# Optimization experiments

Hardware: AMD Instinct MI355X
Metric: run time of the kernel (lower is better)

The kernel has to match this reference:

```python
import jax, jax.numpy as jnp
import numpy as np
import math

N_HEADS = 8
SLOPE = 0.01      # LeakyReLU negative slope (torch default)
EPS_K = 1e-6      # numerical stabilizer in softmax kernel transformation
EPS_N = 1e-5      # GraphNorm eps
TAU = 1.0
N_NODES = 50000
DIM = 64          # in = hidden = out channels (head dim)
M_FEAT = 30       # nb_random_features
N_EDGES = 800000


def softmax_kernel(data, proj, is_query):
    # data: [N, H, D], proj: [M, D] -> [N, H, M] positive random features
    dn = 1.0 / math.sqrt(math.sqrt(data.shape[-1]))
    ratio = 1.0 / math.sqrt(proj.shape[0])
    dd = jnp.einsum('nhd,md->nhm', dn * data, proj)
    diag = jnp.sum(jnp.square(data), axis=-1, keepdims=True) * (dn * dn * 0.5)
    if is_query:
        stab = jnp.max(dd, axis=-1, keepdims=True)            # per (n,h)
    else:
        stab = jnp.max(dd, axis=(0, 2), keepdims=True)        # per h, over n and m
    return ratio * (jnp.exp(dd - diag - stab) + EPS_K)


def nodeformer_conv(x, Wq, bq, Wk, bk, Wv, bv, Wo, bo, proj):
    # x: [N, C]; Wq/Wk/Wv: [C, H*D]; Wo: [H*D, D_out]; proj: [M, D]
    N = x.shape[0]
    H = N_HEADS
    D = Wq.shape[1] // H
    inv = 1.0 / math.sqrt(TAU)
    q = ((x @ Wq + bq).reshape(N, H, D)) * inv
    k = ((x @ Wk + bk).reshape(N, H, D)) * inv
    v = (x @ Wv + bv).reshape(N, H, D)
    qp = softmax_kernel(q, proj, True)    # [N,H,M]
    kp = softmax_kernel(k, proj, False)   # [N,H,M]
    kvs = jnp.einsum('nhm,nhd->hmd', kp, v)          # O(N) linear attention
    num = jnp.einsum('nhm,hmd->nhd', qp, kvs)
    den = jnp.einsum('nhm,hm->nh', qp, jnp.sum(kp, axis=0))
    z = num / den[..., None]                          # [N,H,D]
    return z.reshape(N, H * D) @ Wo + bo


def graph_norm(x, gamma, beta, alpha):
    # single graph: normalize over all nodes; alpha = learnable mean scale
    mu = jnp.mean(x, axis=0, keepdims=True)
    xc = x - alpha * mu
    var = jnp.mean(jnp.square(xc), axis=0, keepdims=True)
    return gamma * xc * jax.lax.rsqrt(var + EPS_N) + beta


def leaky_relu(x):
    return jnp.where(x >= 0, x, SLOPE * x)


def setup_inputs() -> dict:
    key = jax.random.key(0)
    ks = jax.random.split(key, 12)
    HD = N_HEADS * DIM
    s = 0.02
    inp = {
        'patch_embs': jax.random.normal(ks[0], (N_NODES, DIM), jnp.float32),
        'edge_index': jax.random.randint(ks[1], (2, N_EDGES), 0, N_NODES),
        'edge_attr': jax.random.normal(ks[2], (N_EDGES, 8), jnp.float32),
        'Wq': jax.random.normal(ks[3], (3, DIM, HD), jnp.float32) * s,
        'Wk': jax.random.normal(ks[4], (3, DIM, HD), jnp.float32) * s,
        'Wv': jax.random.normal(ks[5], (3, DIM, HD), jnp.float32) * s,
        'Wo': jax.random.normal(ks[6], (3, HD, DIM), jnp.float32) * s,
        'bq': jnp.zeros((3, HD), jnp.float32),
        'bk': jnp.zeros((3, HD), jnp.float32),
        'bv': jnp.zeros((3, HD), jnp.float32),
        'bo': jnp.zeros((3, DIM), jnp.float32),
        'P': jax.random.normal(ks[7], (3, M_FEAT, DIM), jnp.float32),
        'gamma': jnp.ones((3, DIM), jnp.float32),
        'beta': jnp.zeros((3, DIM), jnp.float32),
        'alpha': jnp.ones((3, DIM), jnp.float32),
    }
    return inp


def reference(patch_embs, edge_index, edge_attr, Wq, Wk, Wv, Wo, bq, bk, bv, bo, P, gamma, beta, alpha):
    x = nodeformer_conv(patch_embs, Wq[0], bq[0], Wk[0], bk[0], Wv[0], bv[0], Wo[0], bo[0], P[0])
    x = graph_norm(leaky_relu(x), gamma[0], beta[0], alpha[0])
    x = nodeformer_conv(x, Wq[1], bq[1], Wk[1], bk[1], Wv[1], bv[1], Wo[1], bo[1], P[1])
    x = graph_norm(leaky_relu(x), gamma[1], beta[1], alpha[1])
    x = nodeformer_conv(x, Wq[2], bq[2], Wk[2], bk[2], Wv[2], bv[2], Wo[2], bo[2], P[2])
    x = graph_norm(x, gamma[2], beta[2], alpha[2])
    return x
```

## Files before the change

kernel.cpp:

```cpp
#include <hip/hip_runtime.h>
#include <math.h>


namespace {

constexpr int N    = 50000;
constexpr int C    = 64;
constexpr int H    = 8;
constexpr int HD   = 512;
constexpr int M    = 30;

constexpr int NBK  = 128;
constexpr int NGK  = N / 16;
constexpr int NBQ  = 1024;
constexpr int NGQ8 = N / 8;
constexpr int PSTR = 2016;

__device__ constexpr double DN    = 0.35355339059327373;
__device__ constexpr double RATIO = 0.18257418583505536;
__device__ constexpr double EPSK  = 1e-6;
__device__ constexpr double EPSN  = 1e-5;

__device__ __forceinline__ void kah(double& s, double& c, double v) {
  double y = v - c; double t = s + y; c = (t - s) - y; s = t;
}

__global__ __launch_bounds__(256)
void k_wp(const float* __restrict__ Wk, const float* __restrict__ bk,
          const float* __restrict__ Wq, const float* __restrict__ bq,
          const float* __restrict__ P, float* __restrict__ wp,
          float* __restrict__ bp) {
  const int blk = blockIdx.x, side = blk >> 3, h = blk & 7, t = threadIdx.x;
  const float* W  = side ? Wq : Wk;
  const float* bb = side ? bq : bk;
  for (int s = t; s < 1920; s += 256) {
    const int m = s >> 6, c = s & 63;
    double a = 0.0;
    for (int d = 0; d < 64; ++d)
      a = fma((double)W[c * HD + h * 64 + d], (double)P[m * 64 + d], a);
    wp[((size_t)(side * 8 + h) * 30 + m) * 64 + c] = (float)(a * DN);
  }
  if (t < 30) {
    double a = 0.0;
    for (int d = 0; d < 64; ++d)
      a = fma((double)bb[h * 64 + d], (double)P[t * 64 + d], a);
    bp[(side * 8 + h) * 30 + t] = (float)(a * DN);
  }
}

__global__ __launch_bounds__(256, 4)
void k_kv(const float* __restrict__ x32,
          const float* __restrict__ Wk, const float* __restrict__ bk,
          const float* __restrict__ Wv, const float* __restrict__ bv,
          const float* __restrict__ wp, const float* __restrict__ bp,
          float* __restrict__ partial) {
  __shared__ __align__(16) float wvs[4096];
  __shared__ __align__(16) float wpk[30 * 68];
  __shared__ __align__(16) float xs[16 * 68];
  __shared__ __align__(16) float vsd[16 * 68];
  __shared__ float kplV[480];
  __shared__ float diag[16];
  __shared__ float bpk[30];
  const int t = threadIdx.x, i0 = t >> 6, c0 = t & 63;
  const int h = blockIdx.x >> 7, b = blockIdx.x & (NBK - 1), hb = h * 64;

  for (int s = t; s < 4096; s += 256)
    wvs[s] = Wv[(s >> 6) * HD + hb + (s & 63)];
  for (int s = t; s < 1920; s += 256)
    wpk[(s >> 6) * 68 + (s & 63)] = wp[(size_t)h * 1920 + s];
  if (t < 30) bpk[t] = bp[h * 30 + t];
  const float bk0 = bk[hb + c0], bv0 = bv[hb + c0];
  float acc8[8];
#pragma unroll
  for (int k = 0; k < 8; ++k) acc8[k] = 0.0f;
  float ssv = 0.0f, ses = 0.0f, runmax = -3.0e38f;
  __syncthreads();

  for (int g = b; g < NGK; g += NBK) {
    const int n0 = g * 16;
    __syncthreads();
#pragma unroll
    for (int u = 0; u < 4; ++u)
      xs[(i0 + 4 * u) * 68 + c0] = x32[(size_t)(n0 + i0 + 4 * u) * C + c0];
    __syncthreads();
    float ka[4], va[4];
#pragma unroll
    for (int u = 0; u < 4; ++u) { ka[u] = bk0; va[u] = bv0; }
#pragma unroll 4
    for (int c4 = 0; c4 < 16; ++c4) {
      float4 xv[4];
#pragma unroll
      for (int u = 0; u < 4; ++u)
        xv[u] = reinterpret_cast<const float4*>(xs + (i0 + 4 * u) * 68)[c4];
#pragma unroll
      for (int j = 0; j < 4; ++j) {
        const int c = c4 * 4 + j;
        const float wk_ = Wk[c * HD + hb + c0];
        const float wv_ = wvs[c * 64 + c0];
        const float xj0 = (j == 0) ? xv[0].x : (j == 1) ? xv[0].y : (j == 2) ? xv[0].z : xv[0].w;
        const float xj1 = (j == 0) ? xv[1].x : (j == 1) ? xv[1].y : (j == 2) ? xv[1].z : xv[1].w;
        const float xj2 = (j == 0) ? xv[2].x : (j == 1) ? xv[2].y : (j == 2) ? xv[2].z : xv[2].w;
        const float xj3 = (j == 0) ? xv[3].x : (j == 1) ? xv[3].y : (j == 2) ? xv[3].z : xv[3].w;
        ka[0] = fmaf(xj0, wk_, ka[0]); va[0] = fmaf(xj0, wv_, va[0]);
        ka[1] = fmaf(xj1, wk_, ka[1]); va[1] = fmaf(xj1, wv_, va[1]);
        ka[2] = fmaf(xj2, wk_, ka[2]); va[2] = fmaf(xj2, wv_, va[2]);
        ka[3] = fmaf(xj3, wk_, ka[3]); va[3] = fmaf(xj3, wv_, va[3]);
      }
    }
#pragma unroll
    for (int u = 0; u < 4; ++u) {
      vsd[(i0 + 4 * u) * 68 + c0] = va[u];
      float s = ka[u] * ka[u];
#pragma unroll
      for (int off = 32; off; off >>= 1) s += __shfl_xor(s, off, 64);
      if (c0 == 0) diag[i0 + 4 * u] = s * 0.0625f;
      ssv += va[u];
    }
    __syncthreads();
#pragma unroll
    for (int rep = 0; rep < 2; ++rep) {
      const int item = t + rep * 256;
      if (item < 480) {
        const int di = item / 30, dm = item - di * 30;
        float a = bpk[dm];
#pragma unroll 4
        for (int c4 = 0; c4 < 16; ++c4) {
          const float4 xv = reinterpret_cast<const float4*>(xs + di * 68)[c4];
          const float4 wv = reinterpret_cast<const float4*>(wpk + dm * 68)[c4];
          a = fmaf(xv.x, wv.x, a); a = fmaf(xv.y, wv.y, a);
          a = fmaf(xv.z, wv.z, a); a = fmaf(xv.w, wv.w, a);
        }
        runmax = fmaxf(runmax, a);
        kplV[item] = __expf(a - diag[di]);
      }
    }
    __syncthreads();
    if (t < 30) {
      float gsum = 0.0f;
#pragma unroll
      for (int i = 0; i < 16; ++i) gsum += kplV[i * 30 + t];
      ses += gsum;
    }
    float vr[16];
#pragma unroll
    for (int i = 0; i < 16; ++i) vr[i] = vsd[i * 68 + c0];
#pragma unroll
    for (int k = 0; k < 8; ++k) {
      const int s = t + (k << 8);
      if (s < 1920) {
        const int m = s >> 6;
        float gsum = acc8[k];
#pragma unroll
        for (int i = 0; i < 16; ++i)
          gsum = fmaf(kplV[i * 30 + m], vr[i], gsum);
        acc8[k] = gsum;
      }
    }
  }
  const size_t base = (size_t)blockIdx.x * PSTR;
  __syncthreads();
  xs[t] = ssv;
  vsd[t] = runmax;
  __syncthreads();
  if (t < 64) partial[base + 1950 + t] = xs[t] + xs[t + 64] + xs[t + 128] + xs[t + 192];
  for (int off = 128; off; off >>= 1) {
    if (t < off) vsd[t] = fmaxf(vsd[t], vsd[t + off]);
    __syncthreads();
  }
  if (t == 0) partial[base + 2014] = vsd[0];
  if (t < 30) partial[base + 1920 + t] = ses;
#pragma unroll
  for (int k = 0; k < 8; ++k) {
    const int s = t + (k << 8);
    if (s < 1920) partial[base + s] = acc8[k];
  }
}

__global__ __launch_bounds__(256)
void k_redkv(const float* __restrict__ partial, const float* __restrict__ Wo,
             double* __restrict__ ksumg, float* __restrict__ Gg32) {
  const int h = blockIdx.x, t = threadIdx.x;
  __shared__ float red[256];
  __shared__ double svt[64];
  __shared__ double kvls[M * 64];
  __shared__ double escs;
  const size_t hb = (size_t)h * NBK;
  red[t] = (t < NBK) ? partial[(hb + t) * PSTR + 2014] : -3.0e38f;
  __syncthreads();
  for (int off = 128; off; off >>= 1) {
    if (t < off) red[t] = fmaxf(red[t], red[t + off]);
    __syncthreads();
  }
  if (t == 0) escs = exp(-(double)red[0]);
  __syncthreads();
  const double esc = escs;
  if (t < 64) {
    double s = 0.0;
    for (int b = 0; b < NBK; ++b) s += (double)partial[(hb + b) * PSTR + 1950 + t];
    svt[t] = s;
  } else if (t < 64 + M) {
    const int m = t - 64;
    double s = 0.0;
    for (int b = 0; b < NBK; ++b) s += (double)partial[(hb + b) * PSTR + 1920 + m];
    ksumg[h * M + m] = RATIO * (esc * s + EPSK * (double)N);
  }
  __syncthreads();
#pragma unroll
  for (int k = 0; k < 8; ++k) {
    const int sidx = t + (k << 8);
    if (sidx < M * 64) {
      double s = 0.0;
      for (int b = 0; b < NBK; ++b) s += (double)partial[(hb + b) * PSTR + sidx];
      kvls[sidx] = RATIO * (esc * s + EPSK * svt[sidx & 63]);
    }
  }
  __syncthreads();
#pragma unroll
  for (int k = 0; k < 8; ++k) {
    const int sidx = t + (k << 8);
    if (sidx < M * 64) {
      const int m = sidx >> 6, c = sidx & 63;
      double a = 0.0;
      for (int d = 0; d < 64; ++d)
        a = fma(kvls[m * 64 + d], (double)Wo[(h * 64 + d) * 64 + c], a);
      Gg32[(size_t)h * 1920 + sidx] = (float)a;
    }
  }
}

template <int MODE>
__global__ __launch_bounds__(256, 4)
void k_q(const float* __restrict__ x32,
         const float* __restrict__ Wq, const float* __restrict__ bq,
         const float* __restrict__ wp, const float* __restrict__ bp,
         const double* __restrict__ ksumg, const float* __restrict__ Gg32,
         const float* __restrict__ bo, int do_leaky, int H0,
         double* __restrict__ y, double* __restrict__ psum) {
  __shared__ __align__(16) float wpq[2][30 * 68];
  __shared__ float Gl[2][1920];
  __shared__ __align__(16) float xs[8 * 68];
  __shared__ float qpl[480];
  __shared__ float stabd[16], diagd[16];
  __shared__ double ksl[2][30];
  __shared__ double rdend[16];
  __shared__ float bpq2[2][30];
  __shared__ double red[256];
  const int t = threadIdx.x, i0 = t >> 6, c0 = t & 63;

  for (int s = t; s < 3840; s += 256) {
    const int hh = s / 1920, r = s - hh * 1920, m = r >> 6, c = r & 63;
    wpq[hh][m * 68 + c] = wp[(size_t)(8 + H0 + hh) * 1920 + r];
    Gl[hh][r] = Gg32[(size_t)(H0 + hh) * 1920 + r];
  }
  if (t < 60) {
    ksl[t / 30][t % 30]  = ksumg[(H0 + t / 30) * 30 + (t % 30)];
    bpq2[t / 30][t % 30] = bp[(8 + H0 + t / 30) * 30 + (t % 30)];
  }
  const float bqA = bq[H0 * 64 + c0];
  const float bqB = bq[H0 * 64 + 64 + c0];
  const double bo0 = (double)bo[c0];
  double sy = 0.0, sy2 = 0.0;
  __syncthreads();

  for (int g = blockIdx.x; g < NGQ8; g += NBQ) {
    const int n0 = g * 8;
    __syncthreads();
    xs[i0 * 68 + c0]       = x32[(size_t)(n0 + i0) * C + c0];
    xs[(i0 + 4) * 68 + c0] = x32[(size_t)(n0 + i0 + 4) * C + c0];
    __syncthreads();
    float aq0 = bqA, aq1 = bqB, aq2 = bqA, aq3 = bqB;
#pragma unroll 4
    for (int c4 = 0; c4 < 16; ++c4) {
      const float4 xa = reinterpret_cast<const float4*>(xs + i0 * 68)[c4];
      const float4 xb = reinterpret_cast<const float4*>(xs + (i0 + 4) * 68)[c4];
#pragma unroll
      for (int j = 0; j < 4; ++j) {
        const int c = c4 * 4 + j;
        const float wA = Wq[c * HD + H0 * 64 + c0];
        const float wB = Wq[c * HD + H0 * 64 + 64 + c0];
        const float xaj = (j == 0) ? xa.x : (j == 1) ? xa.y : (j == 2) ? xa.z : xa.w;
        const float xbj = (j == 0) ? xb.x : (j == 1) ? xb.y : (j == 2) ? xb.z : xb.w;
        aq0 = fmaf(xaj, wA, aq0); aq1 = fmaf(xaj, wB, aq1);
        aq2 = fmaf(xbj, wA, aq2); aq3 = fmaf(xbj, wB, aq3);
      }
    }
    {
      float s0 = aq0 * aq0, s1 = aq1 * aq1, s2 = aq2 * aq2, s3 = aq3 * aq3;
#pragma unroll
      for (int off = 32; off; off >>= 1) {
        s0 += __shfl_xor(s0, off, 64); s1 += __shfl_xor(s1, off, 64);
        s2 += __shfl_xor(s2, off, 64); s3 += __shfl_xor(s3, off, 64);
      }
      if (c0 == 0) {
        diagd[i0 * 2]           = s0 * 0.0625f;
        diagd[i0 * 2 + 1]       = s1 * 0.0625f;
        diagd[(i0 + 4) * 2]     = s2 * 0.0625f;
        diagd[(i0 + 4) * 2 + 1] = s3 * 0.0625f;
      }
    }
#pragma unroll
    for (int rep = 0; rep < 2; ++rep) {
      const int item = t + rep * 256;
      if (item < 480) {
        const int i = item / 60, r = item - i * 60, hh = r / 30, m = r - hh * 30;
        float a = bpq2[hh][m];
#pragma unroll 4
        for (int c4 = 0; c4 < 16; ++c4) {
          const float4 xv = reinterpret_cast<const float4*>(xs + i * 68)[c4];
          const float4 wv = reinterpret_cast<const float4*>(wpq[hh] + m * 68)[c4];
          a = fmaf(xv.x, wv.x, a); a = fmaf(xv.y, wv.y, a);
          a = fmaf(xv.z, wv.z, a); a = fmaf(xv.w, wv.w, a);
        }
        qpl[item] = a;
      }
    }
    __syncthreads();
    if (t < 16) {
      const float* q = qpl + t * 30;
      float mx = q[0];
      for (int m = 1; m < 30; ++m) mx = fmaxf(mx, q[m]);
      stabd[t] = mx;
    }
    __syncthreads();
#pragma unroll
    for (int rep = 0; rep < 2; ++rep) {
      const int item = t + rep * 256;
      if (item < 480) {
        const int ih = item / 30;
        qpl[item] = 0.18257418583505536f *
                    (__expf((qpl[item] - diagd[ih]) - stabd[ih]) + 1e-6f);
      }
    }
    __syncthreads();
    if (t < 16) {
      double den = 0.0;
      const float* q = qpl + t * 30;
      const double* ks = ksl[t & 1];
      for (int m = 0; m < 30; ++m) den = fma((double)q[m], ks[m], den);
      rdend[t] = 1.0 / den;
    }
    __syncthreads();
    double acc_a = 0.0, acc_b = 0.0;
#pragma unroll
    for (int hh = 0; hh < 2; ++hh) {
      const float* qa = qpl + (i0 * 2 + hh) * 30;
      const float* qb = qpl + ((i0 + 4) * 2 + hh) * 30;
      const float* g  = Gl[hh] + c0;
      double sa = 0.0, sb = 0.0;
      for (int m = 0; m < 30; ++m) {
        const double gv = (double)g[m * 64];
        sa = fma((double)qa[m], gv, sa);
        sb = fma((double)qb[m], gv, sb);
      }
      acc_a = fma(sa, rdend[i0 * 2 + hh], acc_a);
      acc_b = fma(sb, rdend[(i0 + 4) * 2 + hh], acc_b);
    }
    const size_t ia = (size_t)(n0 + i0) * C + c0;
    const size_t ib = (size_t)(n0 + i0 + 4) * C + c0;
    if (MODE == 0) {
      y[ia] = bo0 + acc_a;
      y[ib] = bo0 + acc_b;
    } else if (MODE == 1) {
      y[ia] += acc_a;
      y[ib] += acc_b;
    } else {
      double va = y[ia] + acc_a, vb = y[ib] + acc_b;
      if (do_leaky) {
        va = (va >= 0.0) ? va : 0.01 * va;
        vb = (vb >= 0.0) ? vb : 0.01 * vb;
      }
      y[ia] = va; y[ib] = vb;
      sy += va + vb;
      sy2 = fma(va, va, sy2);
      sy2 = fma(vb, vb, sy2);
    }
  }
  if (MODE == 2) {
    __syncthreads();
    red[t] = sy;
    __syncthreads();
    if (t < 64) psum[(size_t)blockIdx.x * 128 + t] =
        red[t] + red[t + 64] + red[t + 128] + red[t + 192];
    __syncthreads();
    red[t] = sy2;
    __syncthreads();
    if (t < 64) psum[(size_t)blockIdx.x * 128 + 64 + t] =
        red[t] + red[t + 64] + red[t + 128] + red[t + 192];
  }
}

__global__ void k_norm_params(const double* __restrict__ psum,
                              const float* __restrict__ gamma, const float* __restrict__ beta,
                              const float* __restrict__ alpha, double* __restrict__ nparam) {
  const int t = threadIdx.x;
  __shared__ double m1l[64], m2l[64];
  if (t < 64) {
    double s = 0, c = 0;
    for (int b = 0; b < NBQ; ++b) kah(s, c, psum[(size_t)b * 128 + t]);
    m1l[t] = s - c;
  } else if (t < 128) {
    const int ci = t - 64;
    double s = 0, c = 0;
    for (int b = 0; b < NBQ; ++b) kah(s, c, psum[(size_t)b * 128 + 64 + ci]);
    m2l[ci] = s - c;
  }
  __syncthreads();
  if (t < 64) {
    const double mu = m1l[t] / (double)N;
    const double m2 = m2l[t] / (double)N;
    const double al = (double)alpha[t];
    double var = m2 - (2.0 * al - al * al) * mu * mu;
    if (var < 0.0) var = 0.0;
    nparam[t]       = al * mu;
    nparam[64 + t]  = (double)gamma[t] / sqrt(var + EPSN);
    nparam[128 + t] = (double)beta[t];
  }
}

__global__ void k_cast(const double* __restrict__ yv, const double* __restrict__ nparam,
                       float* __restrict__ dst) {
  const int total = N * C;
  for (int i = blockIdx.x * blockDim.x + threadIdx.x; i < total; i += gridDim.x * blockDim.x) {
    const int c = i & 63;
    dst[i] = (float)((yv[i] - nparam[c]) * nparam[64 + c] + nparam[128 + c]);
  }
}

}

extern "C" void kernel_launch(void* const* d_in, const int* in_sizes, int n_in,
                              void* d_out, int out_size, void* d_ws, size_t ws_size,
                              hipStream_t stream) {
  const float* patch = (const float*)d_in[0];
  const float* Wq = (const float*)d_in[3];
  const float* Wk = (const float*)d_in[4];
  const float* Wv = (const float*)d_in[5];
  const float* Wo = (const float*)d_in[6];
  const float* bq = (const float*)d_in[7];
  const float* bk = (const float*)d_in[8];
  const float* bv = (const float*)d_in[9];
  const float* bo = (const float*)d_in[10];
  const float* P  = (const float*)d_in[11];
  const float* ga = (const float*)d_in[12];
  const float* be = (const float*)d_in[13];
  const float* al = (const float*)d_in[14];
  float* out = (float*)d_out;

  char* wsb = (char*)d_ws;
  double* y      = (double*)wsb;   wsb += (size_t)N * C * 8;
  double* psum   = (double*)wsb;   wsb += (size_t)NBQ * 128 * 8;
  double* nparam = (double*)wsb;   wsb += 192 * 8;
  double* ksumg  = (double*)wsb;   wsb += (size_t)H * M * 8;
  float*  x32    = (float*)wsb;    wsb += (size_t)N * C * 4;
  float*  partial= (float*)wsb;    wsb += (size_t)(H * NBK) * PSTR * 4;
  float*  G32    = (float*)wsb;    wsb += (size_t)H * M * 64 * 4;
  float*  wpf    = (float*)wsb;    wsb += (size_t)2 * H * M * 64 * 4;
  float*  bpf    = (float*)wsb;    wsb += (size_t)2 * H * M * 4;

  for (int L = 0; L < 3; ++L) {
    const float* wq  = Wq + (size_t)L * C * HD;
    const float* wk  = Wk + (size_t)L * C * HD;
    const float* wv  = Wv + (size_t)L * C * HD;
    const float* wo  = Wo + (size_t)L * HD * C;
    const float* bq_ = bq + (size_t)L * HD;
    const float* bk_ = bk + (size_t)L * HD;
    const float* bv_ = bv + (size_t)L * HD;
    const float* bo_ = bo + (size_t)L * C;
    const float* p   = P  + (size_t)L * M * C;
    const int leaky = (L < 2) ? 1 : 0;
    const float* xcur = (L == 0) ? patch : x32;

    k_wp<<<16, 256, 0, stream>>>(wk, bk_, wq, bq_, p, wpf, bpf);
    k_kv<<<H * NBK, 256, 0, stream>>>(xcur, wk, bk_, wv, bv_, wpf, bpf, partial);
    k_redkv<<<H, 256, 0, stream>>>(partial, wo, ksumg, G32);

    k_q<0><<<NBQ, 256, 0, stream>>>(xcur, wq, bq_, wpf, bpf, ksumg, G32, bo_,
                                    leaky, 0, y, psum);
    k_q<1><<<NBQ, 256, 0, stream>>>(xcur, wq, bq_, wpf, bpf, ksumg, G32, bo_,
                                    leaky, 2, y, psum);
    k_q<1><<<NBQ, 256, 0, stream>>>(xcur, wq, bq_, wpf, bpf, ksumg, G32, bo_,
                                    leaky, 4, y, psum);
    k_q<2><<<NBQ, 256, 0, stream>>>(xcur, wq, bq_, wpf, bpf, ksumg, G32, bo_,
                                    leaky, 6, y, psum);

    k_norm_params<<<1, 128, 0, stream>>>(psum, ga + (size_t)L * C, be + (size_t)L * C,
                                         al + (size_t)L * C, nparam);
    k_cast<<<512, 256, 0, stream>>>(y, nparam, (L < 2) ? x32 : out);
  }
}
```

Measured before the change: 2.293 ms.

## Process four heads per query pass and transpose feature buffers in shared memory

The query kernel now handles four heads per launch instead of two, so each layer needs two query launches rather than four and re-reads x and y less often. The MODE 1 accumulate-only path is removed, and MODE 1 now does the final add, optional leaky ReLU and statistics. The G matrix is read straight from global memory instead of being staged in LDS, and the reduction buffer reuses the wpq array, which frees shared memory for the larger four-head projection weights. The random-feature buffers in both kernels are transposed to an m-major layout with unit stride across nodes, which changes LDS access patterns. The cost is higher register pressure from eight accumulators and uncached global G reads inside the inner loop.

```diff
diff --git a/kernel.cpp b/kernel.cpp
--- a/kernel.cpp
+++ b/kernel.cpp
@@ -58,7 +58,7 @@
   __shared__ __align__(16) float wpk[30 * 68];
   __shared__ __align__(16) float xs[16 * 68];
   __shared__ __align__(16) float vsd[16 * 68];
-  __shared__ float kplV[480];
+  __shared__ float kplV[30 * 16];
   __shared__ float diag[16];
   __shared__ float bpk[30];
   const int t = threadIdx.x, i0 = t >> 6, c0 = t & 63;
@@ -121,7 +121,7 @@
     for (int rep = 0; rep < 2; ++rep) {
       const int item = t + rep * 256;
       if (item < 480) {
-        const int di = item / 30, dm = item - di * 30;
+        const int dm = item >> 4, di = item & 15;
         float a = bpk[dm];
 #pragma unroll 4
         for (int c4 = 0; c4 < 16; ++c4) {
@@ -131,14 +131,14 @@
           a = fmaf(xv.z, wv.z, a); a = fmaf(xv.w, wv.w, a);
         }
         runmax = fmaxf(runmax, a);
-        kplV[item] = __expf(a - diag[di]);
+        kplV[dm * 16 + di] = __expf(a - diag[di]);
       }
     }
     __syncthreads();
     if (t < 30) {
       float gsum = 0.0f;
 #pragma unroll
-      for (int i = 0; i < 16; ++i) gsum += kplV[i * 30 + t];
+      for (int i = 0; i < 16; ++i) gsum += kplV[t * 16 + i];
       ses += gsum;
     }
     float vr[16];
@@ -152,7 +152,7 @@
         float gsum = acc8[k];
 #pragma unroll
         for (int i = 0; i < 16; ++i)
-          gsum = fmaf(kplV[i * 30 + m], vr[i], gsum);
+          gsum = fmaf(kplV[m * 16 + i], vr[i], gsum);
         acc8[k] = gsum;
       }
     }
@@ -236,39 +236,39 @@
          const double* __restrict__ ksumg, const float* __restrict__ Gg32,
          const float* __restrict__ bo, int do_leaky, int H0,
          double* __restrict__ y, double* __restrict__ psum) {
-  __shared__ __align__(16) float wpq[2][30 * 68];
-  __shared__ float Gl[2][1920];
+  __shared__ __align__(16) float wpq[4 * 30 * 68];
   __shared__ __align__(16) float xs[8 * 68];
-  __shared__ float qpl[480];
-  __shared__ float stabd[16], diagd[16];
-  __shared__ double ksl[2][30];
-  __shared__ double rdend[16];
-  __shared__ float bpq2[2][30];
-  __shared__ double red[256];
+  __shared__ float  qpl[120 * 8];
+  __shared__ float  stabd[32];
+  __shared__ float  diagd[32];
+  __shared__ double rdend[32];
+  __shared__ double ksl[120];
+  __shared__ float  bpq[120];
   const int t = threadIdx.x, i0 = t >> 6, c0 = t & 63;
 
-  for (int s = t; s < 3840; s += 256) {
-    const int hh = s / 1920, r = s - hh * 1920, m = r >> 6, c = r & 63;
-    wpq[hh][m * 68 + c] = wp[(size_t)(8 + H0 + hh) * 1920 + r];
-    Gl[hh][r] = Gg32[(size_t)(H0 + hh) * 1920 + r];
-  }
-  if (t < 60) {
-    ksl[t / 30][t % 30]  = ksumg[(H0 + t / 30) * 30 + (t % 30)];
-    bpq2[t / 30][t % 30] = bp[(8 + H0 + t / 30) * 30 + (t % 30)];
-  }
-  const float bqA = bq[H0 * 64 + c0];
-  const float bqB = bq[H0 * 64 + 64 + c0];
+  for (int s = t; s < 7680; s += 256) {
+    const int hh = s / 1920, r = s - hh * 1920;
+    wpq[(hh * 30 + (r >> 6)) * 68 + (r & 63)] = wp[(size_t)(8 + H0 + hh) * 1920 + r];
+  }
+  if (t < 120) {
+    ksl[t] = ksumg[H0 * 30 + t];
+    bpq[t] = bp[(8 + H0) * 30 + t];
+  }
+  float bq4[4];
+#pragma unroll
+  for (int hh = 0; hh < 4; ++hh) bq4[hh] = bq[(H0 + hh) * 64 + c0];
   const double bo0 = (double)bo[c0];
   double sy = 0.0, sy2 = 0.0;
   __syncthreads();
 
   for (int g = blockIdx.x; g < NGQ8; g += NBQ) {
     const int n0 = g * 8;
-    __syncthreads();
     xs[i0 * 68 + c0]       = x32[(size_t)(n0 + i0) * C + c0];
     xs[(i0 + 4) * 68 + c0] = x32[(size_t)(n0 + i0 + 4) * C + c0];
     __syncthreads();
-    float aq0 = bqA, aq1 = bqB, aq2 = bqA, aq3 = bqB;
+    float aq[4], ar[4];
+#pragma unroll
+    for (int hh = 0; hh < 4; ++hh) { aq[hh] = bq4[hh]; ar[hh] = bq4[hh]; }
 #pragma unroll 4
     for (int c4 = 0; c4 < 16; ++c4) {
       const float4 xa = reinterpret_cast<const float4*>(xs + i0 * 68)[c4];
@@ -276,38 +276,39 @@
 #pragma unroll
       for (int j = 0; j < 4; ++j) {
         const int c = c4 * 4 + j;
-        const float wA = Wq[c * HD + H0 * 64 + c0];
-        const float wB = Wq[c * HD + H0 * 64 + 64 + c0];
         const float xaj = (j == 0) ? xa.x : (j == 1) ? xa.y : (j == 2) ? xa.z : xa.w;
         const float xbj = (j == 0) ? xb.x : (j == 1) ? xb.y : (j == 2) ? xb.z : xb.w;
-        aq0 = fmaf(xaj, wA, aq0); aq1 = fmaf(xaj, wB, aq1);
-        aq2 = fmaf(xbj, wA, aq2); aq3 = fmaf(xbj, wB, aq3);
-      }
-    }
-    {
-      float s0 = aq0 * aq0, s1 = aq1 * aq1, s2 = aq2 * aq2, s3 = aq3 * aq3;
+#pragma unroll
+        for (int hh = 0; hh < 4; ++hh) {
+          const float w = Wq[c * HD + (H0 + hh) * 64 + c0];
+          aq[hh] = fmaf(xaj, w, aq[hh]);
+          ar[hh] = fmaf(xbj, w, ar[hh]);
+        }
+      }
+    }
+#pragma unroll
+    for (int hh = 0; hh < 4; ++hh) {
+      float s0 = aq[hh] * aq[hh], s1 = ar[hh] * ar[hh];
 #pragma unroll
       for (int off = 32; off; off >>= 1) {
-        s0 += __shfl_xor(s0, off, 64); s1 += __shfl_xor(s1, off, 64);
-        s2 += __shfl_xor(s2, off, 64); s3 += __shfl_xor(s3, off, 64);
+        s0 += __shfl_xor(s0, off, 64);
+        s1 += __shfl_xor(s1, off, 64);
       }
       if (c0 == 0) {
-        diagd[i0 * 2]           = s0 * 0.0625f;
-        diagd[i0 * 2 + 1]       = s1 * 0.0625f;
-        diagd[(i0 + 4) * 2]     = s2 * 0.0625f;
-        diagd[(i0 + 4) * 2 + 1] = s3 * 0.0625f;
-      }
-    }
-#pragma unroll
-    for (int rep = 0; rep < 2; ++rep) {
+        diagd[i0 * 4 + hh]       = s0 * 0.0625f;
+        diagd[(i0 + 4) * 4 + hh] = s1 * 0.0625f;
+      }
+    }
+#pragma unroll
+    for (int rep = 0; rep < 4; ++rep) {
       const int item = t + rep * 256;
-      if (item < 480) {
-        const int i = item / 60, r = item - i * 60, hh = r / 30, m = r - hh * 30;
-        float a = bpq2[hh][m];
+      if (item < 960) {
+        const int j = item >> 3, i = item & 7;
+        float a = bpq[j];
 #pragma unroll 4
         for (int c4 = 0; c4 < 16; ++c4) {
           const float4 xv = reinterpret_cast<const float4*>(xs + i * 68)[c4];
-          const float4 wv = reinterpret_cast<const float4*>(wpq[hh] + m * 68)[c4];
+          const float4 wv = reinterpret_cast<const float4*>(wpq + j * 68)[c4];
           a = fmaf(xv.x, wv.x, a); a = fmaf(xv.y, wv.y, a);
           a = fmaf(xv.z, wv.z, a); a = fmaf(xv.w, wv.w, a);
         }
@@ -315,54 +316,51 @@
       }
     }
     __syncthreads();
-    if (t < 16) {
-      const float* q = qpl + t * 30;
-      float mx = q[0];
-      for (int m = 1; m < 30; ++m) mx = fmaxf(mx, q[m]);
+    if (t < 32) {
+      const int hh = t >> 3, i = t & 7;
+      float mx = qpl[(hh * 30) * 8 + i];
+      for (int m = 1; m < 30; ++m) mx = fmaxf(mx, qpl[(hh * 30 + m) * 8 + i]);
       stabd[t] = mx;
     }
     __syncthreads();
 #pragma unroll
-    for (int rep = 0; rep < 2; ++rep) {
+    for (int rep = 0; rep < 4; ++rep) {
       const int item = t + rep * 256;
-      if (item < 480) {
-        const int ih = item / 30;
+      if (item < 960) {
+        const int j = item >> 3, i = item & 7;
+        const int hh = j / 30;
         qpl[item] = 0.18257418583505536f *
-                    (__expf((qpl[item] - diagd[ih]) - stabd[ih]) + 1e-6f);
-      }
-    }
-    __syncthreads();
-    if (t < 16) {
+                    (__expf((qpl[item] - diagd[i * 4 + hh]) - stabd[hh * 8 + i]) + 1e-6f);
+      }
+    }
+    __syncthreads();
+    if (t < 32) {
+      const int hh = t >> 3, i = t & 7;
       double den = 0.0;
-      const float* q = qpl + t * 30;
-      const double* ks = ksl[t & 1];
-      for (int m = 0; m < 30; ++m) den = fma((double)q[m], ks[m], den);
-      rdend[t] = 1.0 / den;
+      for (int m = 0; m < 30; ++m)
+        den = fma((double)qpl[(hh * 30 + m) * 8 + i], ksl[hh * 30 + m], den);
+      rdend[i * 4 + hh] = 1.0 / den;
     }
     __syncthreads();
     double acc_a = 0.0, acc_b = 0.0;
 #pragma unroll
-    for (int hh = 0; hh < 2; ++hh) {
-      const float* qa = qpl + (i0 * 2 + hh) * 30;
-      const float* qb = qpl + ((i0 + 4) * 2 + hh) * 30;
-      const float* g  = Gl[hh] + c0;
+    for (int hh = 0; hh < 4; ++hh) {
+      const float* g = Gg32 + (size_t)(H0 + hh) * 1920 + c0;
+      const int jb = hh * 30;
       double sa = 0.0, sb = 0.0;
       for (int m = 0; m < 30; ++m) {
         const double gv = (double)g[m * 64];
-        sa = fma((double)qa[m], gv, sa);
-        sb = fma((double)qb[m], gv, sb);
-      }
-      acc_a = fma(sa, rdend[i0 * 2 + hh], acc_a);
-      acc_b = fma(sb, rdend[(i0 + 4) * 2 + hh], acc_b);
+        sa = fma((double)qpl[(jb + m) * 8 + i0], gv, sa);
+        sb = fma((double)qpl[(jb + m) * 8 + i0 + 4], gv, sb);
+      }
+      acc_a = fma(sa, rdend[i0 * 4 + hh], acc_a);
+      acc_b = fma(sb, rdend[(i0 + 4) * 4 + hh], acc_b);
     }
     const size_t ia = (size_t)(n0 + i0) * C + c0;
     const size_t ib = (size_t)(n0 + i0 + 4) * C + c0;
     if (MODE == 0) {
       y[ia] = bo0 + acc_a;
       y[ib] = bo0 + acc_b;
-    } else if (MODE == 1) {
-      y[ia] += acc_a;
-      y[ib] += acc_b;
     } else {
       double va = y[ia] + acc_a, vb = y[ib] + acc_b;
       if (do_leaky) {
@@ -374,8 +372,10 @@
       sy2 = fma(va, va, sy2);
       sy2 = fma(vb, vb, sy2);
     }
-  }
-  if (MODE == 2) {
+    __syncthreads();
+  }
+  if (MODE == 1) {
+    double* red = reinterpret_cast<double*>(wpq);
     __syncthreads();
     red[t] = sy;
     __syncthreads();
@@ -477,11 +477,7 @@
     k_q<0><<<NBQ, 256, 0, stream>>>(xcur, wq, bq_, wpf, bpf, ksumg, G32, bo_,
                                     leaky, 0, y, psum);
     k_q<1><<<NBQ, 256, 0, stream>>>(xcur, wq, bq_, wpf, bpf, ksumg, G32, bo_,
-                                    leaky, 2, y, psum);
-    k_q<1><<<NBQ, 256, 0, stream>>>(xcur, wq, bq_, wpf, bpf, ksumg, G32, bo_,
                                     leaky, 4, y, psum);
-    k_q<2><<<NBQ, 256, 0, stream>>>(xcur, wq, bq_, wpf, bpf, ksumg, G32, bo_,
-                                    leaky, 6, y, psum);
 
     k_norm_params<<<1, 128, 0, stream>>>(psum, ga + (size_t)L * C, be + (size_t)L * C,
                                          al + (size_t)L * C, nparam);
```

Result: slower. 4.799 ms (+109.3%).
